# Kernel optimization log

Hardware: AMD Instinct MI355X
Metric: run time of the kernel (lower is better)

Reference implementation:

```python
import jax, jax.numpy as jnp
import numpy as np

VOCAB = 32000
HID = 1024
B = 16
T = 256


def setup_inputs() -> dict:
    key = jax.random.key(0)
    ks = jax.random.split(key, 16)
    p = lambda k, shape: (jax.random.normal(k, shape, dtype=jnp.float32) * 0.01)
    return {
        "inputs": jax.random.randint(ks[0], (B, T), 0, VOCAB, dtype=jnp.int64),
        "embedding": jax.random.normal(ks[1], (VOCAB, HID), dtype=jnp.float32),
        "W_xi": p(ks[2], (HID, HID)), "W_hi": p(ks[3], (HID, HID)), "b_i": jnp.zeros((HID,), jnp.float32),
        "W_xf": p(ks[4], (HID, HID)), "W_hf": p(ks[5], (HID, HID)), "b_f": jnp.zeros((HID,), jnp.float32),
        "W_xo": p(ks[6], (HID, HID)), "W_ho": p(ks[7], (HID, HID)), "b_o": jnp.zeros((HID,), jnp.float32),
        "W_xc": p(ks[8], (HID, HID)), "W_hc": p(ks[9], (HID, HID)), "b_c": jnp.zeros((HID,), jnp.float32),
        "W_hq": p(ks[10], (HID, VOCAB)), "b_q": jnp.zeros((VOCAB,), jnp.float32),
    }


def _lstm_forward(inputs, embedding, W_xi, W_hi, b_i, W_xf, W_hf, b_f,
                  W_xo, W_ho, b_o, W_xc, W_hc, b_c, W_hq, b_q):
    emb = embedding[inputs]                      # [B, T, H]
    batch, hid = emb.shape[0], embedding.shape[1]
    # fuse the 4 gate weight matrices into single GEMMs (same math, i|f|o|c order)
    Wx = jnp.concatenate([W_xi, W_xf, W_xo, W_xc], axis=1)   # [H, 4H]
    Wh = jnp.concatenate([W_hi, W_hf, W_ho, W_hc], axis=1)   # [H, 4H]
    b = jnp.concatenate([b_i, b_f, b_o, b_c], axis=0)        # [4H]

    def step(carry, x):
        H, C = carry
        g = x @ Wx + H @ Wh + b                  # [B, 4H]
        i, f, o, c = jnp.split(g, 4, axis=1)
        I = jax.nn.sigmoid(i)
        F = jax.nn.sigmoid(f)
        O = jax.nn.sigmoid(o)
        C_tilda = jnp.tanh(c)
        C = F * C + I * C_tilda
        H = O * jnp.tanh(C)
        Y = H @ W_hq + b_q                       # [B, V]
        return (H, C), Y

    H0 = jnp.zeros((batch, hid), emb.dtype)
    C0 = jnp.zeros((batch, hid), emb.dtype)
    (H, C), Ys = jax.lax.scan(step, (H0, C0), jnp.swapaxes(emb, 0, 1))  # Ys: [T, B, V]
    return jnp.swapaxes(Ys, 0, 1), (H, C)


def reference(inputs, embedding, W_xi, W_hi, b_i, W_xf, W_hf, b_f,
              W_xo, W_ho, b_o, W_xc, W_hc, b_c, W_hq, b_q):
    return _lstm_forward(inputs, embedding, W_xi, W_hi, b_i, W_xf, W_hf, b_f,
                         W_xo, W_ho, b_o, W_xc, W_hc, b_c, W_hq, b_q)
```

## Files before the change

### kernel.cpp

```cpp
#include <hip/hip_runtime.h>


typedef __bf16 bf16_t;
typedef bf16_t bf16x8 __attribute__((ext_vector_type(8)));
typedef bf16_t bf16x4 __attribute__((ext_vector_type(4)));
typedef float f32x4 __attribute__((ext_vector_type(4)));
typedef unsigned short u16;
typedef unsigned int u32;
typedef unsigned long long u64;

#define B_ 16
#define T_ 256
#define H_ 1024
#define V_ 32000
#define NWORK 32
#define NCONS 224
#define NSTRIP 500
#define FLAG_STRIDE 16
#define PROG_IDX 512
#define CTL_WORDS 544
#define BSROW 1032

__device__ __forceinline__ u16 f2bf(float x) {
  union { float f; u32 u; } v; v.f = x;
  u32 r = v.u + 0x7FFFu + ((v.u >> 16) & 1u);
  return (u16)(r >> 16);
}
__device__ __forceinline__ bf16x8 ldb8(const u16* p) {
  return *reinterpret_cast<const bf16x8*>(p);
}
__device__ __forceinline__ bf16x8 mk2(const u16* p) {
  bf16x4 lo = *reinterpret_cast<const bf16x4*>(p);
  bf16x4 hi = *reinterpret_cast<const bf16x4*>(p + 64);
  return __builtin_shufflevector(lo, hi, 0, 1, 2, 3, 4, 5, 6, 7);
}
__device__ __forceinline__ float fsig(float x) {
  return __builtin_amdgcn_rcpf(1.0f + __expf(-x));
}
__device__ __forceinline__ float ftanh(float x) {
  float x2 = fminf(fmaxf(2.0f * x, -80.0f), 80.0f);
  float e = __expf(x2);
  return (e - 1.0f) * __builtin_amdgcn_rcpf(e + 1.0f);
}
__device__ __forceinline__ void gll16(const void* g, void* l) {
  __builtin_amdgcn_global_load_lds(
      (const __attribute__((address_space(1))) void*)g,
      (__attribute__((address_space(3))) void*)l, 16, 0, 0);
}
__device__ __forceinline__ u32 ld_agent(const u32* p) {
  return __hip_atomic_load(p, __ATOMIC_RELAXED, __HIP_MEMORY_SCOPE_AGENT);
}
__device__ __forceinline__ void st_agent(u32* p, u32 v) {
  __hip_atomic_store(p, v, __ATOMIC_RELAXED, __HIP_MEMORY_SCOPE_AGENT);
}


__global__ void k_init(u32* Hs0u32, u32* ctl, float* bfu,
                       const float* b0, const float* b1, const float* b2, const float* b3) {
  int i = blockIdx.x * 256 + threadIdx.x;
  if (i < 8192)
    __hip_atomic_store(&Hs0u32[i], 0u, __ATOMIC_RELAXED, __HIP_MEMORY_SCOPE_AGENT);
  if (i < CTL_WORDS)
    st_agent(&ctl[i], 0u);
  if (i < 4096) {
    int g = i >> 10, u = i & 1023;
    const float* bb = (g == 0) ? b0 : (g == 1) ? b1 : (g == 2) ? b2 : b3;
    bfu[i] = bb[u];
  }
}

__global__ void k_embed(const int* __restrict__ ids, const float* __restrict__ emb,
                        u16* __restrict__ out) {
  int r = blockIdx.x;
  int t = r >> 4, b = r & 15;
  int row = ids[b * T_ + t];
  const f32x4 v = *(const f32x4*)&emb[(size_t)row * H_ + threadIdx.x * 4];
  ushort4 o;
  o.x = f2bf(v[0]); o.y = f2bf(v[1]); o.z = f2bf(v[2]); o.w = f2bf(v[3]);
  *(ushort4*)&out[(size_t)r * H_ + threadIdx.x * 4] = o;
}

__global__ void k_fuse8(const float* __restrict__ Wxi, const float* __restrict__ Wxf,
                        const float* __restrict__ Wxo, const float* __restrict__ Wxc,
                        const float* __restrict__ Whi, const float* __restrict__ Whf,
                        const float* __restrict__ Who, const float* __restrict__ Whc,
                        u16* __restrict__ WxT, u16* __restrict__ WhT) {
  __shared__ float ti[64][65];
  int z = blockIdx.z, g = z & 3;
  const float* W;
  if (z < 4) W = (g == 0) ? Wxi : (g == 1) ? Wxf : (g == 2) ? Wxo : Wxc;
  else       W = (g == 0) ? Whi : (g == 1) ? Whf : (g == 2) ? Who : Whc;
  u16* WT = (z < 4) ? WxT : WhT;
  int u0 = blockIdx.x * 64, k0 = blockIdx.y * 64;
  int c = threadIdx.x & 63, rq = threadIdx.x >> 6;
#pragma unroll
  for (int p = 0; p < 16; ++p) {
    int rr = p * 4 + rq;
    ti[rr][c] = W[(size_t)(k0 + rr) * H_ + u0 + c];
  }
  __syncthreads();
#pragma unroll
  for (int p = 0; p < 16; ++p) {
    int uu = p * 4 + rq;
    WT[(size_t)(g * H_ + u0 + uu) * H_ + k0 + c] = f2bf(ti[c][uu]);
  }
}

__global__ void k_transq(const float* __restrict__ Whq, u16* __restrict__ WqT) {
  __shared__ float ti[64][65];
  int n0 = blockIdx.x * 64, k0 = blockIdx.y * 64;
  int c = threadIdx.x & 63, rq = threadIdx.x >> 6;
#pragma unroll
  for (int p = 0; p < 16; ++p) {
    int rr = p * 4 + rq;
    ti[rr][c] = Whq[(size_t)(k0 + rr) * V_ + n0 + c];
  }
  __syncthreads();
#pragma unroll
  for (int p = 0; p < 16; ++p) {
    int nn = p * 4 + rq;
    WqT[(size_t)(n0 + nn) * H_ + k0 + c] = f2bf(ti[c][nn]);
  }
}

__global__ __launch_bounds__(256)
void gemm_gx(const u16* __restrict__ A, const u16* __restrict__ Bt,
             const float* __restrict__ bias, float* __restrict__ out,
             int N, int K) {
  __shared__ u16 As[128 * 32];
  __shared__ u16 Bs[128 * 32];
  const int tid = threadIdx.x;
  const int l = tid & 63, w = tid >> 6;
  const int m0 = blockIdx.y * 128, n0 = blockIdx.x * 128;
  const int wm = (w & 1) * 64, wn = (w >> 1) * 64;
  const int koff = (l >> 4) * 8;

  const int srow = w * 16 + (l >> 2);
  const int scol = (l & 3) * 8;
  const u16* a0p = A + (size_t)(m0 + srow) * K + scol;
  const u16* a1p = A + (size_t)(m0 + 64 + srow) * K + scol;
  const u16* b0p = Bt + (size_t)(n0 + srow) * K + scol;
  const u16* b1p = Bt + (size_t)(n0 + 64 + srow) * K + scol;
  u16* asb0 = As + w * 512;
  u16* asb1 = As + 2048 + w * 512;
  u16* bsb0 = Bs + w * 512;
  u16* bsb1 = Bs + 2048 + w * 512;

  f32x4 acc[4][4] = {};

  for (int k0 = 0; k0 < K; k0 += 32) {
    gll16(a0p + k0, asb0);
    gll16(a1p + k0, asb1);
    gll16(b0p + k0, bsb0);
    gll16(b1p + k0, bsb1);
    asm volatile("s_waitcnt vmcnt(0)" ::: "memory");
    __syncthreads();

    bf16x8 af[4], bfr[4];
#pragma unroll
    for (int tm = 0; tm < 4; ++tm)
      af[tm] = ldb8(&As[(wm + tm * 16 + (l & 15)) * 32 + koff]);
#pragma unroll
    for (int tn = 0; tn < 4; ++tn)
      bfr[tn] = ldb8(&Bs[(wn + tn * 16 + (l & 15)) * 32 + koff]);
#pragma unroll
    for (int tm = 0; tm < 4; ++tm)
#pragma unroll
      for (int tn = 0; tn < 4; ++tn)
        acc[tm][tn] = __builtin_amdgcn_mfma_f32_16x16x32_bf16(af[tm], bfr[tn], acc[tm][tn], 0, 0, 0);
    __syncthreads();
  }

#pragma unroll
  for (int tm = 0; tm < 4; ++tm) {
    int rbase = m0 + wm + tm * 16 + (l >> 4) * 4;
    int t = rbase >> 4;
    int bb = rbase & 15;
#pragma unroll
    for (int tn = 0; tn < 4; ++tn) {
      int n = n0 + wn + tn * 16 + (l & 15);
      float bv = bias[n];
      f32x4 v = acc[tm][tn];
      v[0] += bv; v[1] += bv; v[2] += bv; v[3] += bv;
      *(f32x4*)&out[((size_t)t * N + n) * 16 + bb] = v;
    }
  }
}

__global__ __launch_bounds__(512)
void fused(const u16* __restrict__ WhT, const u16* __restrict__ WqT,
           const float* __restrict__ Gx, u16* __restrict__ Hs,
           u32* __restrict__ ctl, const float* __restrict__ bqv,
           float* __restrict__ out, float* __restrict__ outH, float* __restrict__ outC) {
  __shared__ __align__(16) char ldsbuf[132096];
  const int bid = blockIdx.x;
  const int tid = threadIdx.x, l = tid & 63, w = tid >> 6;

  if (bid < NWORK) {
    float (*gx)[16][16] = (float (*)[16][16])ldsbuf;
    const int wid = bid;
    const int gw = wid * 8 + w;
    const int hu0 = gw * 4;
    const int c = l & 15;
    const int n = (c >> 2) * H_ + hu0 + (c & 3);
    const int koff = (l >> 4) * 8;
    const int kgrp = (l >> 4) * 2;
    const int m = l & 15, u = l >> 4;
    const int hu = hu0 + u;
    const int m4 = m * 4;

    bf16x8 wf[32];
    {
      const u16* bp = WhT + (size_t)n * H_ + koff;
#pragma unroll
      for (int kk = 0; kk < 32; ++kk) wf[kk] = ldb8(bp + kk * 32);
    }

    float Cs = 0.0f;
    u64* HsU64 = (u64*)Hs;
    const u32* myflag = &ctl[(l & 31) * FLAG_STRIDE];

    for (int t = 0; t < T_; ++t) {
      const f32x4 g4 = *(const f32x4*)&Gx[((size_t)t * 4096 + n) * 16 + (size_t)(l >> 4) * 4];

      if (t > 0) {
        if (w == 0) {
          while (true) {
            u32 v = ld_agent(myflag);
            if (__all((int)(v >= (u32)t))) break;
            __builtin_amdgcn_s_sleep(1);
          }
          if (wid == 0 && l == 0) st_agent(&ctl[PROG_IDX], (u32)t);
        }
        __syncthreads();
      }

      const u16* hrow = Hs + (size_t)t * 16384 + m4;
      f32x4 a0 = {}, a1 = {}, a2 = {}, a3 = {};
#pragma unroll
      for (int kk = 0; kk < 32; kk += 4) {
        a0 = __builtin_amdgcn_mfma_f32_16x16x32_bf16(mk2(hrow + (kgrp + (kk + 0) * 8) * 64), wf[kk + 0], a0, 0, 0, 0);
        a1 = __builtin_amdgcn_mfma_f32_16x16x32_bf16(mk2(hrow + (kgrp + (kk + 1) * 8) * 64), wf[kk + 1], a1, 0, 0, 0);
        a2 = __builtin_amdgcn_mfma_f32_16x16x32_bf16(mk2(hrow + (kgrp + (kk + 2) * 8) * 64), wf[kk + 2], a2, 0, 0, 0);
        a3 = __builtin_amdgcn_mfma_f32_16x16x32_bf16(mk2(hrow + (kgrp + (kk + 3) * 8) * 64), wf[kk + 3], a3, 0, 0, 0);
      }
      f32x4 acc = (a0 + a1) + (a2 + a3);

#pragma unroll
      for (int j = 0; j < 4; ++j)
        gx[w][(l >> 4) * 4 + j][c] = acc[j] + g4[j];

      float gi = gx[w][m][0 + u];
      float gf = gx[w][m][4 + u];
      float go = gx[w][m][8 + u];
      float gc = gx[w][m][12 + u];
      float I = fsig(gi);
      float F = fsig(gf);
      float O = fsig(go);
      float Ct = ftanh(gc);
      Cs = F * Cs + I * Ct;
      float Hn = O * ftanh(Cs);

      u32 hb = (u32)f2bf(Hn);
      u32 h1 = __shfl_down(hb, 16);
      u32 h2 = __shfl_down(hb, 32);
      u32 h3 = __shfl_down(hb, 48);
      if (l < 16) {
        u64 pk = (u64)hb | ((u64)h1 << 16) | ((u64)h2 << 32) | ((u64)h3 << 48);
        __hip_atomic_store(&HsU64[(size_t)(t + 1) * 4096 + (size_t)gw * 16 + l], pk,
                           __ATOMIC_RELAXED, __HIP_MEMORY_SCOPE_AGENT);
      }
      if (t == T_ - 1) {
        outH[(size_t)m * H_ + hu] = Hn;
        outC[(size_t)m * H_ + hu] = Cs;
      }

      asm volatile("s_waitcnt vmcnt(0)" ::: "memory");
      __syncthreads();
      if (tid == 0) st_agent(&ctl[wid * FLAG_STRIDE], (u32)(t + 1));
    }

    if (wid == 0 && w == 0) {
      while (true) {
        u32 v = ld_agent(myflag);
        if (__all((int)(v >= (u32)T_))) break;
        __builtin_amdgcn_s_sleep(1);
      }
      if (l == 0) st_agent(&ctl[PROG_IDX], (u32)T_);
    }
    return;
  }

  u16* Bs = (u16*)ldsbuf;
  const int cid = bid - NWORK;
  const int nloc = (w & 3) * 16 + (l & 15);
  const int mhalf = w >> 2;
  const int koff = (l >> 4) * 8;
  const int kgrp = (l >> 4) * 2;
  const int m4 = (l & 15) * 4;
  const size_t tv = (size_t)T_ * V_;

  for (int mt = 0; mt < 32; ++mt) {
    if (tid == 0) {
      const u32 need = (u32)(mt * 8 + 8);
      while (ld_agent(&ctl[PROG_IDX]) < need)
        __builtin_amdgcn_s_sleep(32);
    }
    __syncthreads();

    for (int s = cid; s < NSTRIP; s += NCONS) {
      const int n0 = s * 64;
#pragma unroll
      for (int r8 = 0; r8 < 8; ++r8) {
        int row = w * 8 + r8;
        const u16* src = WqT + (size_t)(n0 + row) * H_;
        u16* dst = Bs + row * BSROW;
        gll16(src + l * 8, dst);
        gll16(src + 512 + l * 8, dst + 512);
      }
      asm volatile("s_waitcnt vmcnt(0)" ::: "memory");
      __syncthreads();

      f32x4 acc[4] = {};
      const u16* hbase = Hs + (size_t)(mt * 8 + mhalf * 4 + 1) * 16384 + m4;
      const u16* bsrow = Bs + nloc * BSROW + koff;
#pragma unroll 4
      for (int kk = 0; kk < 32; ++kk) {
        bf16x8 bf = ldb8(bsrow + kk * 32);
        const int qo = (kgrp + kk * 8) * 64;
        acc[0] = __builtin_amdgcn_mfma_f32_16x16x32_bf16(mk2(hbase + 0 * 16384 + qo), bf, acc[0], 0, 0, 0);
        acc[1] = __builtin_amdgcn_mfma_f32_16x16x32_bf16(mk2(hbase + 1 * 16384 + qo), bf, acc[1], 0, 0, 0);
        acc[2] = __builtin_amdgcn_mfma_f32_16x16x32_bf16(mk2(hbase + 2 * 16384 + qo), bf, acc[2], 0, 0, 0);
        acc[3] = __builtin_amdgcn_mfma_f32_16x16x32_bf16(mk2(hbase + 3 * 16384 + qo), bf, acc[3], 0, 0, 0);
      }

      const int nn = n0 + nloc;
      const float bv = bqv[nn];
#pragma unroll
      for (int tm = 0; tm < 4; ++tm) {
        const int t_glob = mt * 8 + mhalf * 4 + tm;
#pragma unroll
        for (int j = 0; j < 4; ++j) {
          out[(size_t)((l >> 4) * 4 + j) * tv + (size_t)t_glob * V_ + nn] = acc[tm][j] + bv;
        }
      }
      __syncthreads();
    }
  }
}


extern "C" void kernel_launch(void* const* d_in, const int* in_sizes, int n_in,
                              void* d_out, int out_size, void* d_ws, size_t ws_size,
                              hipStream_t stream) {
  const int*   ids = (const int*)d_in[0];
  const float* emb = (const float*)d_in[1];
  const float* Wxi = (const float*)d_in[2];
  const float* Whi = (const float*)d_in[3];
  const float* bi  = (const float*)d_in[4];
  const float* Wxf = (const float*)d_in[5];
  const float* Whf = (const float*)d_in[6];
  const float* bfv = (const float*)d_in[7];
  const float* Wxo = (const float*)d_in[8];
  const float* Who = (const float*)d_in[9];
  const float* bo  = (const float*)d_in[10];
  const float* Wxc = (const float*)d_in[11];
  const float* Whc = (const float*)d_in[12];
  const float* bc  = (const float*)d_in[13];
  const float* Whq = (const float*)d_in[14];
  const float* bq  = (const float*)d_in[15];
  float* out = (float*)d_out;

  char* ws = (char*)d_ws;
  u16* WxT = (u16*)ws;      ws += (size_t)4096 * H_ * 2;
  u16* WhT = (u16*)ws;      ws += (size_t)4096 * H_ * 2;
  u16* WqT = (u16*)ws;      ws += (size_t)V_ * H_ * 2;
  u16* Emb = (u16*)ws;      ws += (size_t)T_ * B_ * H_ * 2;
  float* Gx = (float*)ws;   ws += (size_t)T_ * 4096 * B_ * 4;
  u16* Hs  = (u16*)ws;      ws += (size_t)(T_ + 1) * B_ * H_ * 2;
  float* bfu = (float*)ws;  ws += (size_t)4096 * 4;
  u32* ctl = (u32*)ws;      ws += (size_t)CTL_WORDS * 4;

  k_init<<<64, 256, 0, stream>>>((u32*)Hs, ctl, bfu, bi, bfv, bo, bc);
  k_embed<<<4096, 256, 0, stream>>>(ids, emb, Emb);
  k_fuse8<<<dim3(16, 16, 8), 256, 0, stream>>>(Wxi, Wxf, Wxo, Wxc, Whi, Whf, Who, Whc, WxT, WhT);
  k_transq<<<dim3(500, 16), 256, 0, stream>>>(Whq, WqT);

  gemm_gx<<<dim3(32, 32), 256, 0, stream>>>(Emb, WxT, bfu, Gx, 4096, H_);

  float* outH = out + (size_t)B_ * T_ * V_;
  float* outC = outH + (size_t)B_ * H_;
  fused<<<NWORK + NCONS, 512, 0, stream>>>(WhT, WqT, Gx, Hs, ctl, bq, out, outH, outC);
}
```

Measured before the change: 1.830 ms.

## Fold input-projection GEMM into persistent kernel and reorder vocab projection loops

```diff
diff --git a/kernel.cpp b/kernel.cpp
--- a/kernel.cpp
+++ b/kernel.cpp
@@ -17,8 +17,11 @@
 #define NCONS 224
 #define NSTRIP 500
 #define FLAG_STRIDE 16
-#define PROG_IDX 512
-#define CTL_WORDS 544
+#define FL    0
+#define GXR   512
+#define WQ    1024
+#define PROG  1040
+#define CTL_WORDS 1056
 #define BSROW 1032
 
 __device__ __forceinline__ u16 f2bf(float x) {
@@ -51,6 +54,9 @@
   return __hip_atomic_load(p, __ATOMIC_RELAXED, __HIP_MEMORY_SCOPE_AGENT);
 }
 __device__ __forceinline__ void st_agent(u32* p, u32 v) {
+  __hip_atomic_store(p, v, __ATOMIC_RELAXED, __HIP_MEMORY_SCOPE_AGENT);
+}
+__device__ __forceinline__ void st_agent64(u64* p, u64 v) {
   __hip_atomic_store(p, v, __ATOMIC_RELAXED, __HIP_MEMORY_SCOPE_AGENT);
 }
 
@@ -123,76 +129,15 @@
   }
 }
 
-__global__ __launch_bounds__(256)
-void gemm_gx(const u16* __restrict__ A, const u16* __restrict__ Bt,
-             const float* __restrict__ bias, float* __restrict__ out,
-             int N, int K) {
-  __shared__ u16 As[128 * 32];
-  __shared__ u16 Bs[128 * 32];
-  const int tid = threadIdx.x;
-  const int l = tid & 63, w = tid >> 6;
-  const int m0 = blockIdx.y * 128, n0 = blockIdx.x * 128;
-  const int wm = (w & 1) * 64, wn = (w >> 1) * 64;
-  const int koff = (l >> 4) * 8;
-
-  const int srow = w * 16 + (l >> 2);
-  const int scol = (l & 3) * 8;
-  const u16* a0p = A + (size_t)(m0 + srow) * K + scol;
-  const u16* a1p = A + (size_t)(m0 + 64 + srow) * K + scol;
-  const u16* b0p = Bt + (size_t)(n0 + srow) * K + scol;
-  const u16* b1p = Bt + (size_t)(n0 + 64 + srow) * K + scol;
-  u16* asb0 = As + w * 512;
-  u16* asb1 = As + 2048 + w * 512;
-  u16* bsb0 = Bs + w * 512;
-  u16* bsb1 = Bs + 2048 + w * 512;
-
-  f32x4 acc[4][4] = {};
-
-  for (int k0 = 0; k0 < K; k0 += 32) {
-    gll16(a0p + k0, asb0);
-    gll16(a1p + k0, asb1);
-    gll16(b0p + k0, bsb0);
-    gll16(b1p + k0, bsb1);
-    asm volatile("s_waitcnt vmcnt(0)" ::: "memory");
-    __syncthreads();
-
-    bf16x8 af[4], bfr[4];
-#pragma unroll
-    for (int tm = 0; tm < 4; ++tm)
-      af[tm] = ldb8(&As[(wm + tm * 16 + (l & 15)) * 32 + koff]);
-#pragma unroll
-    for (int tn = 0; tn < 4; ++tn)
-      bfr[tn] = ldb8(&Bs[(wn + tn * 16 + (l & 15)) * 32 + koff]);
-#pragma unroll
-    for (int tm = 0; tm < 4; ++tm)
-#pragma unroll
-      for (int tn = 0; tn < 4; ++tn)
-        acc[tm][tn] = __builtin_amdgcn_mfma_f32_16x16x32_bf16(af[tm], bfr[tn], acc[tm][tn], 0, 0, 0);
-    __syncthreads();
-  }
-
-#pragma unroll
-  for (int tm = 0; tm < 4; ++tm) {
-    int rbase = m0 + wm + tm * 16 + (l >> 4) * 4;
-    int t = rbase >> 4;
-    int bb = rbase & 15;
-#pragma unroll
-    for (int tn = 0; tn < 4; ++tn) {
-      int n = n0 + wn + tn * 16 + (l & 15);
-      float bv = bias[n];
-      f32x4 v = acc[tm][tn];
-      v[0] += bv; v[1] += bv; v[2] += bv; v[3] += bv;
-      *(f32x4*)&out[((size_t)t * N + n) * 16 + bb] = v;
-    }
-  }
-}
-
 __global__ __launch_bounds__(512)
-void fused(const u16* __restrict__ WhT, const u16* __restrict__ WqT,
-           const float* __restrict__ Gx, u16* __restrict__ Hs,
-           u32* __restrict__ ctl, const float* __restrict__ bqv,
-           float* __restrict__ out, float* __restrict__ outH, float* __restrict__ outC) {
+void fused(const u16* __restrict__ WhT, const u16* __restrict__ WxT,
+           const u16* __restrict__ WqT, const u16* __restrict__ Emb,
+           float* __restrict__ Gx, u16* __restrict__ Hs,
+           u32* __restrict__ ctl, const float* __restrict__ bfu,
+           const float* __restrict__ bqv, float* __restrict__ out,
+           float* __restrict__ outH, float* __restrict__ outC) {
   __shared__ __align__(16) char ldsbuf[132096];
+  __shared__ u32 s_tk;
   const int bid = blockIdx.x;
   const int tid = threadIdx.x, l = tid & 63, w = tid >> 6;
 
@@ -218,21 +163,22 @@
 
     float Cs = 0.0f;
     u64* HsU64 = (u64*)Hs;
-    const u32* myflag = &ctl[(l & 31) * FLAG_STRIDE];
+    const u32* myflag = &ctl[FL + (l & 31) * FLAG_STRIDE];
 
     for (int t = 0; t < T_; ++t) {
+      if ((t & 7) == 0) {
+        while (ld_agent(&ctl[GXR + (t >> 3) * FLAG_STRIDE]) < 32u)
+          __builtin_amdgcn_s_sleep(2);
+      }
       const f32x4 g4 = *(const f32x4*)&Gx[((size_t)t * 4096 + n) * 16 + (size_t)(l >> 4) * 4];
 
       if (t > 0) {
-        if (w == 0) {
-          while (true) {
-            u32 v = ld_agent(myflag);
-            if (__all((int)(v >= (u32)t))) break;
-            __builtin_amdgcn_s_sleep(1);
-          }
-          if (wid == 0 && l == 0) st_agent(&ctl[PROG_IDX], (u32)t);
+        while (true) {
+          u32 v = ld_agent(myflag);
+          if (__all((int)(v >= (u32)t))) break;
+          __builtin_amdgcn_s_sleep(2);
         }
-        __syncthreads();
+        if (gw == 0 && l == 0) st_agent(&ctl[PROG], (u32)t);
       }
 
       const u16* hrow = Hs + (size_t)t * 16384 + m4;
@@ -267,8 +213,7 @@
       u32 h3 = __shfl_down(hb, 48);
       if (l < 16) {
         u64 pk = (u64)hb | ((u64)h1 << 16) | ((u64)h2 << 32) | ((u64)h3 << 48);
-        __hip_atomic_store(&HsU64[(size_t)(t + 1) * 4096 + (size_t)gw * 16 + l], pk,
-                           __ATOMIC_RELAXED, __HIP_MEMORY_SCOPE_AGENT);
+        st_agent64(&HsU64[(size_t)(t + 1) * 4096 + (size_t)gw * 16 + l], pk);
       }
       if (t == T_ - 1) {
         outH[(size_t)m * H_ + hu] = Hn;
@@ -277,36 +222,98 @@
 
       asm volatile("s_waitcnt vmcnt(0)" ::: "memory");
       __syncthreads();
-      if (tid == 0) st_agent(&ctl[wid * FLAG_STRIDE], (u32)(t + 1));
+      if (tid == 0) st_agent(&ctl[FL + wid * FLAG_STRIDE], (u32)(t + 1));
     }
 
-    if (wid == 0 && w == 0) {
+    if (gw == 0) {
       while (true) {
         u32 v = ld_agent(myflag);
         if (__all((int)(v >= (u32)T_))) break;
-        __builtin_amdgcn_s_sleep(1);
-      }
-      if (l == 0) st_agent(&ctl[PROG_IDX], (u32)T_);
+        __builtin_amdgcn_s_sleep(2);
+      }
+      if (l == 0) st_agent(&ctl[PROG], (u32)T_);
     }
     return;
   }
 
-  u16* Bs = (u16*)ldsbuf;
   const int cid = bid - NWORK;
-  const int nloc = (w & 3) * 16 + (l & 15);
-  const int mhalf = w >> 2;
-  const int koff = (l >> 4) * 8;
-  const int kgrp = (l >> 4) * 2;
-  const int m4 = (l & 15) * 4;
-  const size_t tv = (size_t)T_ * V_;
-
-  for (int mt = 0; mt < 32; ++mt) {
-    if (tid == 0) {
-      const u32 need = (u32)(mt * 8 + 8);
-      while (ld_agent(&ctl[PROG_IDX]) < need)
-        __builtin_amdgcn_s_sleep(32);
+
+  {
+    u16* As = (u16*)ldsbuf;
+    u16* Bs = As + 4096;
+    const int wm = (w & 1) * 64, wn = (w >> 1) * 32;
+    const int koff = (l >> 4) * 8;
+    const int srow = tid >> 2;
+    const int scol = (tid & 3) * 8;
+    u16* dstA = As + (size_t)w * 512;
+    u16* dstB = Bs + (size_t)w * 512;
+
+    for (;;) {
+      __syncthreads();
+      if (tid == 0)
+        s_tk = __hip_atomic_fetch_add(&ctl[WQ], 1u, __ATOMIC_RELAXED, __HIP_MEMORY_SCOPE_AGENT);
+      __syncthreads();
+      u32 tk = s_tk;
+      if (tk >= 1024u) break;
+      const int mt = (int)(tk >> 5), nt = (int)(tk & 31);
+      const int m0 = mt * 128, n0 = nt * 128;
+      const u16* srcA = Emb + (size_t)(m0 + srow) * H_ + scol;
+      const u16* srcB = WxT + (size_t)(n0 + srow) * H_ + scol;
+
+      f32x4 acc[4][2] = {};
+      for (int k0 = 0; k0 < H_; k0 += 32) {
+        gll16(srcA + k0, dstA);
+        gll16(srcB + k0, dstB);
+        asm volatile("s_waitcnt vmcnt(0)" ::: "memory");
+        __syncthreads();
+        bf16x8 af[4], bfr[2];
+#pragma unroll
+        for (int tm = 0; tm < 4; ++tm)
+          af[tm] = ldb8(&As[(wm + tm * 16 + (l & 15)) * 32 + koff]);
+#pragma unroll
+        for (int tn = 0; tn < 2; ++tn)
+          bfr[tn] = ldb8(&Bs[(wn + tn * 16 + (l & 15)) * 32 + koff]);
+#pragma unroll
+        for (int tm = 0; tm < 4; ++tm)
+#pragma unroll
+          for (int tn = 0; tn < 2; ++tn)
+            acc[tm][tn] = __builtin_amdgcn_mfma_f32_16x16x32_bf16(af[tm], bfr[tn], acc[tm][tn], 0, 0, 0);
+        __syncthreads();
+      }
+
+#pragma unroll
+      for (int tm = 0; tm < 4; ++tm) {
+        int rbase = m0 + wm + tm * 16 + (l >> 4) * 4;
+        int t = rbase >> 4;
+        int bb = rbase & 15;
+#pragma unroll
+        for (int tn = 0; tn < 2; ++tn) {
+          int nn = n0 + wn + tn * 16 + (l & 15);
+          float bv = bfu[nn];
+          union { float f[2]; u64 u; } p0, p1;
+          p0.f[0] = acc[tm][tn][0] + bv; p0.f[1] = acc[tm][tn][1] + bv;
+          p1.f[0] = acc[tm][tn][2] + bv; p1.f[1] = acc[tm][tn][3] + bv;
+          u64* o = (u64*)&Gx[((size_t)t * 4096 + nn) * 16 + bb];
+          st_agent64(&o[0], p0.u);
+          st_agent64(&o[1], p1.u);
+        }
+      }
+      asm volatile("s_waitcnt vmcnt(0)" ::: "memory");
+      __syncthreads();
+      if (tid == 0)
+        __hip_atomic_fetch_add(&ctl[GXR + mt * FLAG_STRIDE], 1u, __ATOMIC_RELAXED, __HIP_MEMORY_SCOPE_AGENT);
     }
-    __syncthreads();
+  }
+  __syncthreads();
+
+  {
+    u16* Bs = (u16*)ldsbuf;
+    const int nloc = (w & 3) * 16 + (l & 15);
+    const int mhalf = w >> 2;
+    const int koff = (l >> 4) * 8;
+    const int kgrp = (l >> 4) * 2;
+    const int m4 = (l & 15) * 4;
+    const size_t tv = (size_t)T_ * V_;
 
     for (int s = cid; s < NSTRIP; s += NCONS) {
       const int n0 = s * 64;
@@ -321,27 +328,37 @@
       asm volatile("s_waitcnt vmcnt(0)" ::: "memory");
       __syncthreads();
 
-      f32x4 acc[4] = {};
-      const u16* hbase = Hs + (size_t)(mt * 8 + mhalf * 4 + 1) * 16384 + m4;
       const u16* bsrow = Bs + nloc * BSROW + koff;
-#pragma unroll 4
-      for (int kk = 0; kk < 32; ++kk) {
-        bf16x8 bf = ldb8(bsrow + kk * 32);
-        const int qo = (kgrp + kk * 8) * 64;
-        acc[0] = __builtin_amdgcn_mfma_f32_16x16x32_bf16(mk2(hbase + 0 * 16384 + qo), bf, acc[0], 0, 0, 0);
-        acc[1] = __builtin_amdgcn_mfma_f32_16x16x32_bf16(mk2(hbase + 1 * 16384 + qo), bf, acc[1], 0, 0, 0);
-        acc[2] = __builtin_amdgcn_mfma_f32_16x16x32_bf16(mk2(hbase + 2 * 16384 + qo), bf, acc[2], 0, 0, 0);
-        acc[3] = __builtin_amdgcn_mfma_f32_16x16x32_bf16(mk2(hbase + 3 * 16384 + qo), bf, acc[3], 0, 0, 0);
-      }
-
       const int nn = n0 + nloc;
       const float bv = bqv[nn];
-#pragma unroll
-      for (int tm = 0; tm < 4; ++tm) {
-        const int t_glob = mt * 8 + mhalf * 4 + tm;
-#pragma unroll
-        for (int j = 0; j < 4; ++j) {
-          out[(size_t)((l >> 4) * 4 + j) * tv + (size_t)t_glob * V_ + nn] = acc[tm][j] + bv;
+
+      for (int mt = 0; mt < 32; ++mt) {
+        if (tid == 0) {
+          const u32 need = (u32)(mt * 8 + 8);
+          while (ld_agent(&ctl[PROG]) < need)
+            __builtin_amdgcn_s_sleep(16);
+        }
+        __syncthreads();
+
+        f32x4 acc[4] = {};
+        const u16* hbase = Hs + (size_t)(mt * 8 + mhalf * 4 + 1) * 16384 + m4;
+#pragma unroll 4
+        for (int kk = 0; kk < 32; ++kk) {
+          bf16x8 bf = ldb8(bsrow + kk * 32);
+          const int qo = (kgrp + kk * 8) * 64;
+          acc[0] = __builtin_amdgcn_mfma_f32_16x16x32_bf16(mk2(hbase + 0 * 16384 + qo), bf, acc[0], 0, 0, 0);
+          acc[1] = __builtin_amdgcn_mfma_f32_16x16x32_bf16(mk2(hbase + 1 * 16384 + qo), bf, acc[1], 0, 0, 0);
+          acc[2] = __builtin_amdgcn_mfma_f32_16x16x32_bf16(mk2(hbase + 2 * 16384 + qo), bf, acc[2], 0, 0, 0);
+          acc[3] = __builtin_amdgcn_mfma_f32_16x16x32_bf16(mk2(hbase + 3 * 16384 + qo), bf, acc[3], 0, 0, 0);
+        }
+
+#pragma unroll
+        for (int tm = 0; tm < 4; ++tm) {
+          const int t_glob = mt * 8 + mhalf * 4 + tm;
+#pragma unroll
+          for (int j = 0; j < 4; ++j) {
+            out[(size_t)((l >> 4) * 4 + j) * tv + (size_t)t_glob * V_ + nn] = acc[tm][j] + bv;
+          }
         }
       }
       __syncthreads();
@@ -386,9 +403,8 @@
   k_fuse8<<<dim3(16, 16, 8), 256, 0, stream>>>(Wxi, Wxf, Wxo, Wxc, Whi, Whf, Who, Whc, WxT, WhT);
   k_transq<<<dim3(500, 16), 256, 0, stream>>>(Whq, WqT);
 
-  gemm_gx<<<dim3(32, 32), 256, 0, stream>>>(Emb, WxT, bfu, Gx, 4096, H_);
-
   float* outH = out + (size_t)B_ * T_ * V_;
   float* outC = outH + (size_t)B_ * H_;
-  fused<<<NWORK + NCONS, 512, 0, stream>>>(WhT, WqT, Gx, Hs, ctl, bq, out, outH, outC);
-}
+  fused<<<NWORK + NCONS, 512, 0, stream>>>(WhT, WxT, WqT, Emb, Gx, Hs, ctl, bfu, bq,
+                                           out, outH, outC);
+}
```

Result: slower. 2.576 ms (+40.7%).
